# Performance work log

Hardware: AMD Instinct MI355X
Metric: run time of the kernel (lower is better)

## Reference

```python
import jax, jax.numpy as jnp
import numpy as np

N_NODES = 50000
N_EDGES = 600000
D_IN = 128
D_OUT = 128
BN_EPS = 1e-5


def batchnorm(h, gamma, beta):
    # training-mode BatchNorm1d over the node (batch) axis
    mean = jnp.mean(h, axis=0)
    var = jnp.var(h, axis=0)
    return (h - mean) * jax.lax.rsqrt(var + BN_EPS) * gamma + beta


def setup_inputs() -> dict:
    key = jax.random.key(0)
    ks = jax.random.split(key, 6)
    x = jax.random.normal(ks[0], (N_NODES, D_IN), dtype=jnp.float32)
    edge_index = jax.random.randint(ks[1], (2, N_EDGES), 0, N_NODES, dtype=jnp.int64)
    s_in = 1.0 / np.sqrt(D_IN)
    s_out = 1.0 / np.sqrt(D_OUT)
    return {
        "x": x,
        "edge_index": edge_index,
        "W_mlp": jax.random.normal(ks[2], (D_IN, D_OUT), dtype=jnp.float32) * s_in,
        "b_mlp": jax.random.normal(ks[3], (D_OUT,), dtype=jnp.float32) * s_in,
        "gamma1": jnp.ones((D_OUT,), dtype=jnp.float32),
        "beta1": jnp.zeros((D_OUT,), dtype=jnp.float32),
        "W_conv": jax.random.normal(ks[4], (D_OUT, D_OUT), dtype=jnp.float32) * s_out,
        "b_conv": jax.random.normal(ks[5], (D_OUT,), dtype=jnp.float32) * s_out,
        "gamma2": jnp.ones((D_OUT,), dtype=jnp.float32),
        "beta2": jnp.zeros((D_OUT,), dtype=jnp.float32),
    }


def reference(x, edge_index, W_mlp, b_mlp, gamma1, beta1, W_conv, b_conv, gamma2, beta2):
    N = x.shape[0]
    # MLP: Linear -> BatchNorm1d -> ReLU
    h = x @ W_mlp + b_mlp
    h = jax.nn.relu(batchnorm(h, gamma1, beta1))

    # GCNConv with add_self_loops=True, normalize=True (symmetric deg^-1/2)
    loops = jnp.arange(N, dtype=edge_index.dtype)
    src = jnp.concatenate([edge_index[0], loops])  # [E+N]
    dst = jnp.concatenate([edge_index[1], loops])

    h = h @ W_conv  # [N, D_OUT], bias applied after aggregation (PyG semantics)

    ones = jnp.ones(dst.shape[0], dtype=h.dtype)
    deg = jax.ops.segment_sum(ones, dst, num_segments=N)  # degree at targets
    dinv = jnp.where(deg > 0, jax.lax.rsqrt(deg), 0.0)
    norm = dinv[src] * dinv[dst]  # [E+N]

    msgs = norm[:, None] * h[src]  # gather + scale
    out = jax.ops.segment_sum(msgs, dst, num_segments=N) + b_conv

    # trailing BatchNorm + ReLU (act is truthy)
    return jax.nn.relu(batchnorm(out, gamma2, beta2))
```

## Files before the change

kernel.cpp:

```cpp
#include <hip/hip_runtime.h>
#include <math.h>

#define N_NODES 50000
#define N_EDGES 600000
#define D 128
#define BN_EPS 1e-5f
#define ELLW 64
#define NREP 16

typedef float f32x4 __attribute__((ext_vector_type(4)));
typedef short short8 __attribute__((ext_vector_type(8)));

__device__ __forceinline__ unsigned short f2bf(float f) {
    unsigned int x = __float_as_uint(f);
    return (unsigned short)((x + 0x7FFFu + ((x >> 16) & 1u)) >> 16);
}

__global__ void prep_kernel(const float* __restrict__ W1, const float* __restrict__ W2,
                            unsigned short* __restrict__ WT1, unsigned short* __restrict__ WT2,
                            int* __restrict__ cur, float* __restrict__ stats) {
    int idx = blockIdx.x * blockDim.x + threadIdx.x;
    if (idx < D * D) {
        int col = idx >> 7, k = idx & 127;
        WT1[col * D + k] = f2bf(W1[k * D + col]);
        WT2[col * D + k] = f2bf(W2[k * D + col]);
    }
    if (idx < N_NODES) cur[idx] = 0;
    if (idx < NREP * 4 * D) stats[idx] = 0.0f;
}

__global__ void scatter_kernel(const int* __restrict__ srcI, const int* __restrict__ dstI,
                               int* __restrict__ cur, int* __restrict__ ell) {
    int e = blockIdx.x * blockDim.x + threadIdx.x;
    if (e >= N_EDGES) return;
    int d = dstI[e];
    int pos = atomicAdd(&cur[d], 1);
    if (pos < ELLW) ell[(size_t)d * ELLW + pos] = srcI[e];
}

template<bool BN, bool HAS_BIAS, bool STATS, bool IN_BF16, bool OUT_BF16>
__global__ __launch_bounds__(256, 2) void gemm_ws_kernel(
    const float* __restrict__ Af, const unsigned short* __restrict__ Ab,
    const unsigned short* __restrict__ WT,
    const float* __restrict__ bn_sum, const float* __restrict__ bn_sq,
    const float* __restrict__ bn_gamma, const float* __restrict__ bn_beta,
    const float* __restrict__ out_bias, float* __restrict__ C,
    unsigned short* __restrict__ Cb, int M,
    float* __restrict__ sum_out, float* __restrict__ sq_out)
{
    __shared__ __align__(16) float scs[D];
    __shared__ __align__(16) float bis[D];
    __shared__ float ssum[D];
    __shared__ float ssq[D];

    const int tid  = threadIdx.x;
    const int lane = tid & 63;
    const int w    = tid >> 6;
    const int l15  = lane & 15;
    const int lg   = lane >> 4;

    if (BN) {
        if (tid < D) {
            float s = 0.f, q = 0.f;
            #pragma unroll
            for (int r = 0; r < NREP; ++r) { s += bn_sum[r * D + tid]; q += bn_sq[r * D + tid]; }
            const float inv_n = 1.0f / (float)N_NODES;
            float mean = s * inv_n;
            float var  = q * inv_n - mean * mean;
            float rstd = rsqrtf(var + BN_EPS);
            float sc = bn_gamma[tid] * rstd;
            scs[tid] = sc;
            bis[tid] = bn_beta[tid] - mean * sc;
        }
    }
    if (STATS) {
        if (tid < D) { ssum[tid] = 0.f; ssq[tid] = 0.f; }
    }
    if (BN || STATS) __syncthreads();

    short8 b[8][4];
    #pragma unroll
    for (int ct = 0; ct < 8; ++ct)
        #pragma unroll
        for (int ks = 0; ks < 4; ++ks)
            b[ct][ks] = *(const short8*)&WT[(size_t)(ct * 16 + l15) * D + ks * 32 + lg * 8];

    float ob[8];
    #pragma unroll
    for (int ct = 0; ct < 8; ++ct) ob[ct] = HAS_BIAS ? out_bias[ct * 16 + l15] : 0.f;

    float psum[8], psq[8];
    #pragma unroll
    for (int ct = 0; ct < 8; ++ct) { psum[ct] = 0.f; psq[ct] = 0.f; }

    const int nt = (M + 15) / 16;
    for (int t = blockIdx.x * 4 + w; t < nt; t += gridDim.x * 4) {
        int ar = t * 16 + l15; if (ar > M - 1) ar = M - 1;
        short8 af[4];
        #pragma unroll
        for (int ks = 0; ks < 4; ++ks) {
            const int kb = ks * 32 + lg * 8;
            float vv[8];
            if (IN_BF16) {
                short8 raw = *(const short8*)&Ab[(size_t)ar * D + kb];
                #pragma unroll
                for (int j = 0; j < 8; ++j)
                    vv[j] = __uint_as_float(((unsigned)(unsigned short)raw[j]) << 16);
            } else {
                const float* ap = &Af[(size_t)ar * D + kb];
                float4 v0 = *(const float4*)ap;
                float4 v1 = *(const float4*)(ap + 4);
                vv[0] = v0.x; vv[1] = v0.y; vv[2] = v0.z; vv[3] = v0.w;
                vv[4] = v1.x; vv[5] = v1.y; vv[6] = v1.z; vv[7] = v1.w;
            }
            short8 a8;
            #pragma unroll
            for (int j = 0; j < 8; ++j) {
                float f = vv[j];
                if (BN) f = fmaxf(fmaf(f, scs[kb + j], bis[kb + j]), 0.f);
                a8[j] = (short)f2bf(f);
            }
            af[ks] = a8;
        }

        f32x4 acc[8];
        #pragma unroll
        for (int ct = 0; ct < 8; ++ct) acc[ct] = (f32x4){0.f, 0.f, 0.f, 0.f};
        #pragma unroll
        for (int ks = 0; ks < 4; ++ks)
            #pragma unroll
            for (int ct = 0; ct < 8; ++ct)
                acc[ct] = __builtin_amdgcn_mfma_f32_16x16x32_bf16(af[ks], b[ct][ks], acc[ct], 0, 0, 0);

        const int rb2 = t * 16 + lg * 4;
        #pragma unroll
        for (int j = 0; j < 4; ++j) {
            const int row = rb2 + j;
            if (row < M) {
                #pragma unroll
                for (int ct = 0; ct < 8; ++ct) {
                    float o = acc[ct][j] + ob[ct];
                    if (OUT_BF16) Cb[(size_t)row * D + ct * 16 + l15] = f2bf(o);
                    else          C[(size_t)row * D + ct * 16 + l15] = o;
                    if (STATS) { psum[ct] += o; psq[ct] = fmaf(o, o, psq[ct]); }
                }
            }
        }
    }

    if (STATS) {
        #pragma unroll
        for (int ct = 0; ct < 8; ++ct) {
            atomicAdd(&ssum[ct * 16 + l15], psum[ct]);
            atomicAdd(&ssq[ct * 16 + l15], psq[ct]);
        }
        __syncthreads();
        const int rep = (blockIdx.x & (NREP - 1)) * D;
        if (tid < D) {
            unsafeAtomicAdd(&sum_out[rep + tid], ssum[tid]);
            unsafeAtomicAdd(&sq_out[rep + tid], ssq[tid]);
        }
    }
}

__device__ __forceinline__ void bfp(unsigned pv, float& fx, float& fy) {
    fx = __uint_as_float(pv << 16);
    fy = __uint_as_float(pv & 0xFFFF0000u);
}

__global__ __launch_bounds__(256) void gather_kernel(
    const int* __restrict__ ell, const int* __restrict__ cnt,
    const unsigned short* __restrict__ h2b,
    const float* __restrict__ b_conv, float* __restrict__ outpre,
    float* __restrict__ sum_out, float* __restrict__ sq_out)
{
    const int lane = threadIdx.x & 63;
    const int wid  = threadIdx.x >> 6;
    const int col  = lane * 2;
    const float2 bc = *(const float2*)&b_conv[col];
    float2 sum = make_float2(0.f, 0.f);
    float2 sq  = make_float2(0.f, 0.f);

    for (int d0 = blockIdx.x * 8 + wid * 2; d0 < N_NODES; d0 += gridDim.x * 8) {
        const int d1 = d0 + 1;
        int cAr = cnt[d0];
        int cBr = cnt[d1];
        const float ddA = rsqrtf((float)cAr + 1.0f);
        const float ddB = rsqrtf((float)cBr + 1.0f);
        int cA = cAr > ELLW ? ELLW : cAr;
        int cB = cBr > ELLW ? ELLW : cBr;
        float hAx, hAy, hBx, hBy;
        bfp(*(const unsigned*)&h2b[(size_t)d0 * D + col], hAx, hAy);
        bfp(*(const unsigned*)&h2b[(size_t)d1 * D + col], hBx, hBy);
        float2 accA, accB;
        accA.x = ddA * hAx; accA.y = ddA * hAy;
        accB.x = ddB * hBx; accB.y = ddB * hBy;

        int slA = 0, slB = 0;
        float wlA = 0.f, wlB = 0.f;
        if (lane < cA) { slA = ell[(size_t)d0 * ELLW + lane]; wlA = rsqrtf((float)cnt[slA] + 1.0f); }
        if (lane < cB) { slB = ell[(size_t)d1 * ELLW + lane]; wlB = rsqrtf((float)cnt[slB] + 1.0f); }

        const int cmin = cA < cB ? cA : cB;
        int j = 0;
        for (; j + 4 <= cmin; j += 4) {
            unsigned pA[4], pB[4];
            float wA[4], wB[4];
            #pragma unroll
            for (int u = 0; u < 4; ++u) {
                int sA = __shfl(slA, j + u);
                int sB = __shfl(slB, j + u);
                wA[u] = __shfl(wlA, j + u);
                wB[u] = __shfl(wlB, j + u);
                pA[u] = *(const unsigned*)&h2b[(size_t)sA * D + col];
                pB[u] = *(const unsigned*)&h2b[(size_t)sB * D + col];
            }
            #pragma unroll
            for (int u = 0; u < 4; ++u) {
                float ax, ay, bx, by;
                bfp(pA[u], ax, ay);
                bfp(pB[u], bx, by);
                accA.x = fmaf(wA[u], ax, accA.x);
                accA.y = fmaf(wA[u], ay, accA.y);
                accB.x = fmaf(wB[u], bx, accB.x);
                accB.y = fmaf(wB[u], by, accB.y);
            }
        }
        int jA = j, jB = j;
        for (; jA < cA; ++jA) {
            int s = __shfl(slA, jA);
            float ww = __shfl(wlA, jA);
            float ax, ay;
            bfp(*(const unsigned*)&h2b[(size_t)s * D + col], ax, ay);
            accA.x = fmaf(ww, ax, accA.x);
            accA.y = fmaf(ww, ay, accA.y);
        }
        for (; jB < cB; ++jB) {
            int s = __shfl(slB, jB);
            float ww = __shfl(wlB, jB);
            float bx, by;
            bfp(*(const unsigned*)&h2b[(size_t)s * D + col], bx, by);
            accB.x = fmaf(ww, bx, accB.x);
            accB.y = fmaf(ww, by, accB.y);
        }

        float2 oA, oB;
        oA.x = fmaf(ddA, accA.x, bc.x);
        oA.y = fmaf(ddA, accA.y, bc.y);
        oB.x = fmaf(ddB, accB.x, bc.x);
        oB.y = fmaf(ddB, accB.y, bc.y);
        *(float2*)&outpre[(size_t)d0 * D + col] = oA;
        *(float2*)&outpre[(size_t)d1 * D + col] = oB;
        sum.x += oA.x + oB.x; sum.y += oA.y + oB.y;
        sq.x = fmaf(oA.x, oA.x, sq.x); sq.x = fmaf(oB.x, oB.x, sq.x);
        sq.y = fmaf(oA.y, oA.y, sq.y); sq.y = fmaf(oB.y, oB.y, sq.y);
    }

    __shared__ float2 sS[256];
    __shared__ float2 qS[256];
    sS[threadIdx.x] = sum; qS[threadIdx.x] = sq;
    __syncthreads();
    if (wid == 0) {
        #pragma unroll
        for (int w = 1; w < 4; ++w) {
            float2 s2 = sS[w * 64 + lane];
            float2 q2 = qS[w * 64 + lane];
            sum.x += s2.x; sum.y += s2.y;
            sq.x += q2.x; sq.y += q2.y;
        }
        const int rep = (blockIdx.x & (NREP - 1)) * D;
        unsafeAtomicAdd(&sum_out[rep + col + 0], sum.x);
        unsafeAtomicAdd(&sum_out[rep + col + 1], sum.y);
        unsafeAtomicAdd(&sq_out[rep + col + 0], sq.x);
        unsafeAtomicAdd(&sq_out[rep + col + 1], sq.y);
    }
}

__global__ void final_kernel(float* __restrict__ out,
        const float* __restrict__ s_sum, const float* __restrict__ s_sq,
        const float* __restrict__ gamma, const float* __restrict__ beta) {
    __shared__ __align__(16) float scs[D];
    __shared__ __align__(16) float bis[D];
    const int tid = threadIdx.x;
    if (tid < D) {
        float s = 0.f, q = 0.f;
        #pragma unroll
        for (int r = 0; r < NREP; ++r) { s += s_sum[r * D + tid]; q += s_sq[r * D + tid]; }
        const float inv_n = 1.0f / (float)N_NODES;
        float mean = s * inv_n;
        float var  = q * inv_n - mean * mean;
        float rstd = rsqrtf(var + BN_EPS);
        float sc = gamma[tid] * rstd;
        scs[tid] = sc;
        bis[tid] = beta[tid] - mean * sc;
    }
    __syncthreads();
    const int t = blockIdx.x * blockDim.x + tid;
    const int c4 = t & 31;
    float4 sc = *(const float4*)&scs[c4 * 4];
    float4 bi = *(const float4*)&bis[c4 * 4];
    const int total = N_NODES * D / 4;
    const int stride = gridDim.x * blockDim.x;
    for (int i = t; i < total; i += stride) {
        float4 v = ((const float4*)out)[i];
        v.x = fmaxf(fmaf(v.x, sc.x, bi.x), 0.f);
        v.y = fmaxf(fmaf(v.y, sc.y, bi.y), 0.f);
        v.z = fmaxf(fmaf(v.z, sc.z, bi.z), 0.f);
        v.w = fmaxf(fmaf(v.w, sc.w, bi.w), 0.f);
        ((float4*)out)[i] = v;
    }
}

extern "C" void kernel_launch(void* const* d_in, const int* in_sizes, int n_in,
                              void* d_out, int out_size, void* d_ws, size_t ws_size,
                              hipStream_t stream) {
    const float* x      = (const float*)d_in[0];
    const int*   edge   = (const int*)d_in[1];
    const float* W_mlp  = (const float*)d_in[2];
    const float* b_mlp  = (const float*)d_in[3];
    const float* gamma1 = (const float*)d_in[4];
    const float* beta1  = (const float*)d_in[5];
    const float* W_conv = (const float*)d_in[6];
    const float* b_conv = (const float*)d_in[7];
    const float* gamma2 = (const float*)d_in[8];
    const float* beta2  = (const float*)d_in[9];
    float* out = (float*)d_out;

    float* ws = (float*)d_ws;
    unsigned short* h1b = (unsigned short*)ws;
    unsigned short* h2b = (unsigned short*)(ws + (size_t)N_NODES * D / 2);
    int*   ell  = (int*)h1b;
    float* extra = ws + (size_t)N_NODES * D;
    int*   cur  = (int*)extra;
    float* stats = extra + N_NODES;
    float* sum1 = stats;                  float* sq1 = stats + NREP * D;
    float* sum2 = stats + 2 * NREP * D;   float* sq2 = stats + 3 * NREP * D;
    unsigned short* WT1 = (unsigned short*)(stats + 4 * NREP * D);
    unsigned short* WT2 = WT1 + D * D;

    const int* srcI = edge;
    const int* dstI = edge + N_EDGES;

    prep_kernel<<<(N_NODES + 255) / 256, 256, 0, stream>>>(W_mlp, W_conv, WT1, WT2, cur, stats);

    gemm_ws_kernel<false, true, true, false, true><<<392, 256, 0, stream>>>(
        x, nullptr, WT1, nullptr, nullptr, nullptr, nullptr, b_mlp, nullptr, h1b, N_NODES, sum1, sq1);

    gemm_ws_kernel<true, false, false, true, true><<<392, 256, 0, stream>>>(
        nullptr, h1b, WT2, sum1, sq1, gamma1, beta1, nullptr, nullptr, h2b, N_NODES, nullptr, nullptr);

    scatter_kernel<<<(N_EDGES + 255) / 256, 256, 0, stream>>>(srcI, dstI, cur, ell);

    gather_kernel<<<1024, 256, 0, stream>>>(ell, cur, h2b, b_conv, out, sum2, sq2);

    final_kernel<<<2048, 256, 0, stream>>>(out, sum2, sq2, gamma2, beta2);
}
```

Baseline: 213.6 us.

## Fuse ELL scatter into first GEMM launch and give ELL its own buffer

Edge scatter into the ELL adjacency now runs as extra blocks inside the first GEMM launch, so the scatter overlaps with the GEMM instead of running as a separate kernel after the second GEMM. To make this legal, the workspace is re-laid out so ELL no longer aliases the h1 buffer. GEMM templates are split into two specialized kernels, and the gather grid is doubled. The cost is more workspace memory, and the scatter blocks compete with the GEMM blocks for the same compute units.

```diff
diff --git a/kernel.cpp b/kernel.cpp
--- a/kernel.cpp
+++ b/kernel.cpp
@@ -7,6 +7,7 @@
 #define BN_EPS 1e-5f
 #define ELLW 64
 #define NREP 16
+#define GEMM1_BLOCKS 392
 
 typedef float f32x4 __attribute__((ext_vector_type(4)));
 typedef short short8 __attribute__((ext_vector_type(8)));
@@ -29,54 +30,35 @@
     if (idx < NREP * 4 * D) stats[idx] = 0.0f;
 }
 
-__global__ void scatter_kernel(const int* __restrict__ srcI, const int* __restrict__ dstI,
-                               int* __restrict__ cur, int* __restrict__ ell) {
-    int e = blockIdx.x * blockDim.x + threadIdx.x;
-    if (e >= N_EDGES) return;
-    int d = dstI[e];
-    int pos = atomicAdd(&cur[d], 1);
-    if (pos < ELLW) ell[(size_t)d * ELLW + pos] = srcI[e];
-}
-
-template<bool BN, bool HAS_BIAS, bool STATS, bool IN_BF16, bool OUT_BF16>
-__global__ __launch_bounds__(256, 2) void gemm_ws_kernel(
-    const float* __restrict__ Af, const unsigned short* __restrict__ Ab,
-    const unsigned short* __restrict__ WT,
-    const float* __restrict__ bn_sum, const float* __restrict__ bn_sq,
-    const float* __restrict__ bn_gamma, const float* __restrict__ bn_beta,
-    const float* __restrict__ out_bias, float* __restrict__ C,
-    unsigned short* __restrict__ Cb, int M,
-    float* __restrict__ sum_out, float* __restrict__ sq_out)
+__global__ __launch_bounds__(256, 2) void gemm1_scatter_kernel(
+    const float* __restrict__ A, const unsigned short* __restrict__ WT,
+    const float* __restrict__ out_bias, unsigned short* __restrict__ Cb, int M,
+    float* __restrict__ sum_out, float* __restrict__ sq_out,
+    const int* __restrict__ srcI, const int* __restrict__ dstI,
+    int* __restrict__ cur, int* __restrict__ ell)
 {
-    __shared__ __align__(16) float scs[D];
-    __shared__ __align__(16) float bis[D];
+    const int tid = threadIdx.x;
+
+    if (blockIdx.x >= GEMM1_BLOCKS) {
+        int e = (blockIdx.x - GEMM1_BLOCKS) * 256 + tid;
+        if (e < N_EDGES) {
+            int d = dstI[e];
+            int pos = atomicAdd(&cur[d], 1);
+            if (pos < ELLW) ell[(size_t)d * ELLW + pos] = srcI[e];
+        }
+        return;
+    }
+
     __shared__ float ssum[D];
     __shared__ float ssq[D];
 
-    const int tid  = threadIdx.x;
     const int lane = tid & 63;
     const int w    = tid >> 6;
     const int l15  = lane & 15;
     const int lg   = lane >> 4;
 
-    if (BN) {
-        if (tid < D) {
-            float s = 0.f, q = 0.f;
-            #pragma unroll
-            for (int r = 0; r < NREP; ++r) { s += bn_sum[r * D + tid]; q += bn_sq[r * D + tid]; }
-            const float inv_n = 1.0f / (float)N_NODES;
-            float mean = s * inv_n;
-            float var  = q * inv_n - mean * mean;
-            float rstd = rsqrtf(var + BN_EPS);
-            float sc = bn_gamma[tid] * rstd;
-            scs[tid] = sc;
-            bis[tid] = bn_beta[tid] - mean * sc;
-        }
-    }
-    if (STATS) {
-        if (tid < D) { ssum[tid] = 0.f; ssq[tid] = 0.f; }
-    }
-    if (BN || STATS) __syncthreads();
+    if (tid < D) { ssum[tid] = 0.f; ssq[tid] = 0.f; }
+    __syncthreads();
 
     short8 b[8][4];
     #pragma unroll
@@ -87,39 +69,26 @@
 
     float ob[8];
     #pragma unroll
-    for (int ct = 0; ct < 8; ++ct) ob[ct] = HAS_BIAS ? out_bias[ct * 16 + l15] : 0.f;
+    for (int ct = 0; ct < 8; ++ct) ob[ct] = out_bias[ct * 16 + l15];
 
     float psum[8], psq[8];
     #pragma unroll
     for (int ct = 0; ct < 8; ++ct) { psum[ct] = 0.f; psq[ct] = 0.f; }
 
     const int nt = (M + 15) / 16;
-    for (int t = blockIdx.x * 4 + w; t < nt; t += gridDim.x * 4) {
+    for (int t = blockIdx.x * 4 + w; t < nt; t += GEMM1_BLOCKS * 4) {
         int ar = t * 16 + l15; if (ar > M - 1) ar = M - 1;
         short8 af[4];
         #pragma unroll
         for (int ks = 0; ks < 4; ++ks) {
             const int kb = ks * 32 + lg * 8;
-            float vv[8];
-            if (IN_BF16) {
-                short8 raw = *(const short8*)&Ab[(size_t)ar * D + kb];
-                #pragma unroll
-                for (int j = 0; j < 8; ++j)
-                    vv[j] = __uint_as_float(((unsigned)(unsigned short)raw[j]) << 16);
-            } else {
-                const float* ap = &Af[(size_t)ar * D + kb];
-                float4 v0 = *(const float4*)ap;
-                float4 v1 = *(const float4*)(ap + 4);
-                vv[0] = v0.x; vv[1] = v0.y; vv[2] = v0.z; vv[3] = v0.w;
-                vv[4] = v1.x; vv[5] = v1.y; vv[6] = v1.z; vv[7] = v1.w;
-            }
+            const float* ap = &A[(size_t)ar * D + kb];
+            float4 v0 = *(const float4*)ap;
+            float4 v1 = *(const float4*)(ap + 4);
+            float vv[8] = {v0.x, v0.y, v0.z, v0.w, v1.x, v1.y, v1.z, v1.w};
             short8 a8;
             #pragma unroll
-            for (int j = 0; j < 8; ++j) {
-                float f = vv[j];
-                if (BN) f = fmaxf(fmaf(f, scs[kb + j], bis[kb + j]), 0.f);
-                a8[j] = (short)f2bf(f);
-            }
+            for (int j = 0; j < 8; ++j) a8[j] = (short)f2bf(vv[j]);
             af[ks] = a8;
         }
 
@@ -140,25 +109,98 @@
                 #pragma unroll
                 for (int ct = 0; ct < 8; ++ct) {
                     float o = acc[ct][j] + ob[ct];
-                    if (OUT_BF16) Cb[(size_t)row * D + ct * 16 + l15] = f2bf(o);
-                    else          C[(size_t)row * D + ct * 16 + l15] = o;
-                    if (STATS) { psum[ct] += o; psq[ct] = fmaf(o, o, psq[ct]); }
+                    Cb[(size_t)row * D + ct * 16 + l15] = f2bf(o);
+                    psum[ct] += o; psq[ct] = fmaf(o, o, psq[ct]);
                 }
             }
         }
     }
 
-    if (STATS) {
-        #pragma unroll
-        for (int ct = 0; ct < 8; ++ct) {
-            atomicAdd(&ssum[ct * 16 + l15], psum[ct]);
-            atomicAdd(&ssq[ct * 16 + l15], psq[ct]);
-        }
-        __syncthreads();
-        const int rep = (blockIdx.x & (NREP - 1)) * D;
-        if (tid < D) {
-            unsafeAtomicAdd(&sum_out[rep + tid], ssum[tid]);
-            unsafeAtomicAdd(&sq_out[rep + tid], ssq[tid]);
+    #pragma unroll
+    for (int ct = 0; ct < 8; ++ct) {
+        atomicAdd(&ssum[ct * 16 + l15], psum[ct]);
+        atomicAdd(&ssq[ct * 16 + l15], psq[ct]);
+    }
+    __syncthreads();
+    const int rep = (blockIdx.x & (NREP - 1)) * D;
+    if (tid < D) {
+        unsafeAtomicAdd(&sum_out[rep + tid], ssum[tid]);
+        unsafeAtomicAdd(&sq_out[rep + tid], ssq[tid]);
+    }
+}
+
+__global__ __launch_bounds__(256, 2) void gemm2_kernel(
+    const unsigned short* __restrict__ Ab, const unsigned short* __restrict__ WT,
+    const float* __restrict__ bn_sum, const float* __restrict__ bn_sq,
+    const float* __restrict__ bn_gamma, const float* __restrict__ bn_beta,
+    unsigned short* __restrict__ Cb, int M)
+{
+    __shared__ __align__(16) float scs[D];
+    __shared__ __align__(16) float bis[D];
+
+    const int tid  = threadIdx.x;
+    const int lane = tid & 63;
+    const int w    = tid >> 6;
+    const int l15  = lane & 15;
+    const int lg   = lane >> 4;
+
+    if (tid < D) {
+        float s = 0.f, q = 0.f;
+        #pragma unroll
+        for (int r = 0; r < NREP; ++r) { s += bn_sum[r * D + tid]; q += bn_sq[r * D + tid]; }
+        const float inv_n = 1.0f / (float)N_NODES;
+        float mean = s * inv_n;
+        float var  = q * inv_n - mean * mean;
+        float rstd = rsqrtf(var + BN_EPS);
+        float sc = bn_gamma[tid] * rstd;
+        scs[tid] = sc;
+        bis[tid] = bn_beta[tid] - mean * sc;
+    }
+    __syncthreads();
+
+    short8 b[8][4];
+    #pragma unroll
+    for (int ct = 0; ct < 8; ++ct)
+        #pragma unroll
+        for (int ks = 0; ks < 4; ++ks)
+            b[ct][ks] = *(const short8*)&WT[(size_t)(ct * 16 + l15) * D + ks * 32 + lg * 8];
+
+    const int nt = (M + 15) / 16;
+    for (int t = blockIdx.x * 4 + w; t < nt; t += gridDim.x * 4) {
+        int ar = t * 16 + l15; if (ar > M - 1) ar = M - 1;
+        short8 af[4];
+        #pragma unroll
+        for (int ks = 0; ks < 4; ++ks) {
+            const int kb = ks * 32 + lg * 8;
+            short8 raw = *(const short8*)&Ab[(size_t)ar * D + kb];
+            short8 a8;
+            #pragma unroll
+            for (int j = 0; j < 8; ++j) {
+                float f = __uint_as_float(((unsigned)(unsigned short)raw[j]) << 16);
+                f = fmaxf(fmaf(f, scs[kb + j], bis[kb + j]), 0.f);
+                a8[j] = (short)f2bf(f);
+            }
+            af[ks] = a8;
+        }
+
+        f32x4 acc[8];
+        #pragma unroll
+        for (int ct = 0; ct < 8; ++ct) acc[ct] = (f32x4){0.f, 0.f, 0.f, 0.f};
+        #pragma unroll
+        for (int ks = 0; ks < 4; ++ks)
+            #pragma unroll
+            for (int ct = 0; ct < 8; ++ct)
+                acc[ct] = __builtin_amdgcn_mfma_f32_16x16x32_bf16(af[ks], b[ct][ks], acc[ct], 0, 0, 0);
+
+        const int rb2 = t * 16 + lg * 4;
+        #pragma unroll
+        for (int j = 0; j < 4; ++j) {
+            const int row = rb2 + j;
+            if (row < M) {
+                #pragma unroll
+                for (int ct = 0; ct < 8; ++ct)
+                    Cb[(size_t)row * D + ct * 16 + l15] = f2bf(acc[ct][j]);
+            }
         }
     }
 }
@@ -326,13 +368,11 @@
     const float* beta2  = (const float*)d_in[9];
     float* out = (float*)d_out;
 
-    float* ws = (float*)d_ws;
-    unsigned short* h1b = (unsigned short*)ws;
-    unsigned short* h2b = (unsigned short*)(ws + (size_t)N_NODES * D / 2);
-    int*   ell  = (int*)h1b;
-    float* extra = ws + (size_t)N_NODES * D;
-    int*   cur  = (int*)extra;
-    float* stats = extra + N_NODES;
+    unsigned short* h1b = (unsigned short*)d_ws;
+    unsigned short* h2b = h1b + (size_t)N_NODES * D;
+    int*   ell  = (int*)(h2b + (size_t)N_NODES * D);
+    int*   cur  = ell + (size_t)N_NODES * ELLW;
+    float* stats = (float*)(cur + N_NODES);
     float* sum1 = stats;                  float* sq1 = stats + NREP * D;
     float* sum2 = stats + 2 * NREP * D;   float* sq2 = stats + 3 * NREP * D;
     unsigned short* WT1 = (unsigned short*)(stats + 4 * NREP * D);
@@ -343,15 +383,14 @@
 
     prep_kernel<<<(N_NODES + 255) / 256, 256, 0, stream>>>(W_mlp, W_conv, WT1, WT2, cur, stats);
 
-    gemm_ws_kernel<false, true, true, false, true><<<392, 256, 0, stream>>>(
-        x, nullptr, WT1, nullptr, nullptr, nullptr, nullptr, b_mlp, nullptr, h1b, N_NODES, sum1, sq1);
-
-    gemm_ws_kernel<true, false, false, true, true><<<392, 256, 0, stream>>>(
-        nullptr, h1b, WT2, sum1, sq1, gamma1, beta1, nullptr, nullptr, h2b, N_NODES, nullptr, nullptr);
-
-    scatter_kernel<<<(N_EDGES + 255) / 256, 256, 0, stream>>>(srcI, dstI, cur, ell);
-
-    gather_kernel<<<1024, 256, 0, stream>>>(ell, cur, h2b, b_conv, out, sum2, sq2);
+    const int scatter_blocks = (N_EDGES + 255) / 256;
+    gemm1_scatter_kernel<<<GEMM1_BLOCKS + scatter_blocks, 256, 0, stream>>>(
+        x, WT1, b_mlp, h1b, N_NODES, sum1, sq1, srcI, dstI, cur, ell);
+
+    gemm2_kernel<<<392, 256, 0, stream>>>(
+        h1b, WT2, sum1, sq1, gamma1, beta1, h2b, N_NODES);
+
+    gather_kernel<<<2048, 256, 0, stream>>>(ell, cur, h2b, b_conv, out, sum2, sq2);
 
     final_kernel<<<2048, 256, 0, stream>>>(out, sum2, sq2, gamma2, beta2);
 }
```

After: 192.1 us. 10.1% less time.
